# Kernel tuning notes

Hardware: AMD Instinct MI355X
Metric: run time of the kernel (lower is better)

## Reference

```python
import jax, jax.numpy as jnp
import numpy as np

B, T, V, D, H, C = 64, 512, 50000, 128, 256, 50


def setup_inputs() -> dict:
    key = jax.random.key(0)
    ks = jax.random.split(key, 15)
    s = 0.05
    rn = lambda k, shape: jax.random.normal(k, shape, jnp.float32) * s
    words = jax.random.randint(ks[0], (B, T), 0, V)
    target = jax.random.randint(ks[1], (B, T), 0, C)
    seq_len = jax.random.randint(ks[2], (B,), T // 2, T + 1)
    seq_len = seq_len.at[0].set(T)  # ensure at least one full-length sequence
    return dict(
        words=words, target=target, seq_len=seq_len,
        emb=rn(ks[3], (V, D)),
        W_ih_f=rn(ks[4], (4 * H, D)), W_hh_f=rn(ks[5], (4 * H, H)), b_f=rn(ks[6], (4 * H,)),
        W_ih_b=rn(ks[7], (4 * H, D)), W_hh_b=rn(ks[8], (4 * H, H)), b_b=rn(ks[9], (4 * H,)),
        fc_W=rn(ks[10], (C, 2 * H)), fc_b=rn(ks[11], (C,)),
        trans=rn(ks[12], (C, C)), start_s=rn(ks[13], (C,)), end_s=rn(ks[14], (C,)),
    )


def _lstm(x, W_ih, W_hh, b):
    # unidirectional LSTM, PyTorch gate order (i, f, g, o). x: [B,T,D] -> h: [B,T,H]
    Hh = W_hh.shape[1]
    xg = jnp.einsum('btd,gd->btg', x, W_ih) + b  # [B,T,4H]

    def step(carry, xt):
        h, c = carry
        g = xt + h @ W_hh.T
        i, f, gg, o = jnp.split(g, 4, axis=-1)
        c = jax.nn.sigmoid(f) * c + jax.nn.sigmoid(i) * jnp.tanh(gg)
        h = jax.nn.sigmoid(o) * jnp.tanh(c)
        return (h, c), h

    h0 = jnp.zeros((x.shape[0], Hh), x.dtype)
    _, hs = jax.lax.scan(step, (h0, h0), jnp.swapaxes(xg, 0, 1))
    return jnp.swapaxes(hs, 0, 1)


def _rev_idx(seq_len, t_len):
    # per-sequence time-reversal indices (packed-sequence semantics for the backward LSTM)
    t = jnp.arange(t_len)[None, :]
    L = seq_len[:, None]
    return jnp.where(t < L, L - 1 - t, t)


def _bilstm_crf_loss(words, target, seq_len, emb, W_ih_f, W_hh_f, b_f,
                     W_ih_b, W_hh_b, b_b, fc_W, fc_b, trans, start_s, end_s):
    x = emb[words]  # [B,T,D]
    h_f = _lstm(x, W_ih_f, W_hh_f, b_f)
    idx = _rev_idx(seq_len, x.shape[1])
    x_rev = jnp.take_along_axis(x, idx[:, :, None], axis=1)
    h_b = jnp.take_along_axis(_lstm(x_rev, W_ih_b, W_hh_b, b_b), idx[:, :, None], axis=1)
    feats = jnp.concatenate([h_f, h_b], axis=-1) @ fc_W.T + fc_b  # [B,T,C]
    logits = jax.nn.log_softmax(feats, axis=-1)
    mask = jnp.arange(x.shape[1])[None, :] < seq_len[:, None]  # [B,T] bool

    # --- CRF normalizer (forward algorithm) ---
    alpha0 = logits[:, 0] + start_s  # [B,C]

    def step(alpha, inp):
        emit_t, m_t = inp  # [B,C], [B]
        tmp = alpha[:, :, None] + trans[None, :, :] + emit_t[:, None, :]
        new = jax.nn.logsumexp(tmp, axis=1)
        return jnp.where(m_t[:, None], new, alpha), None

    alpha, _ = jax.lax.scan(step, alpha0,
                            (jnp.swapaxes(logits, 0, 1)[1:], jnp.swapaxes(mask, 0, 1)[1:]))
    norm = jax.nn.logsumexp(alpha + end_s, axis=1)  # [B]

    # --- gold path score ---
    maskf = mask.astype(logits.dtype)
    emit = jnp.take_along_axis(logits, target[:, :, None], axis=2)[..., 0]  # [B,T]
    trans_sc = trans[target[:, :-1], target[:, 1:]]  # [B,T-1]
    last = target[jnp.arange(target.shape[0]), seq_len - 1]
    gold = (emit * maskf).sum(1) + (trans_sc * maskf[:, 1:]).sum(1) \
           + start_s[target[:, 0]] + end_s[last]

    return jnp.mean(norm - gold)


def reference(words, target, seq_len, emb, W_ih_f, W_hh_f, b_f,
              W_ih_b, W_hh_b, b_b, fc_W, fc_b, trans, start_s, end_s):
    return _bilstm_crf_loss(words, target, seq_len, emb, W_ih_f, W_hh_f, b_f,
                            W_ih_b, W_hh_b, b_b, fc_W, fc_b, trans, start_s, end_s)
```

## Files before the change

kernel.cpp:

```cpp
#include <hip/hip_runtime.h>
#include <hip/hip_bf16.h>

#define BB 64
#define TT 512
#define DD 128
#define HH 256
#define G4 1024
#define CC 50

typedef __bf16 bf16x8 __attribute__((ext_vector_type(8)));
typedef float  f32x4  __attribute__((ext_vector_type(4)));
typedef _Float16 h16x2 __attribute__((ext_vector_type(2)));

#if defined(__has_builtin)
#if __has_builtin(__builtin_amdgcn_fdot2)
#define HAS_FDOT2 1
#endif
#endif

__device__ __forceinline__ float bl16(unsigned u) { return __uint_as_float(u << 16); }
__device__ __forceinline__ float bh16(unsigned u) { return __uint_as_float(u & 0xffff0000u); }

__device__ __forceinline__ float sigf(float x) {
    return 1.f / (1.f + __expf(-x));
}
__device__ __forceinline__ float tanh_s(float x) {
    float ax = fabsf(x);
    float e = __expf(-2.f * ax);
    float r = (1.f - e) / (1.f + e);
    return copysignf(r, x);
}

__device__ __forceinline__ float dot8(float acc, uint4 w, uint4 h) {
#ifdef HAS_FDOT2
    acc = __builtin_amdgcn_fdot2(__builtin_bit_cast(h16x2, w.x),
                                 __builtin_bit_cast(h16x2, h.x), acc, false);
    acc = __builtin_amdgcn_fdot2(__builtin_bit_cast(h16x2, w.y),
                                 __builtin_bit_cast(h16x2, h.y), acc, false);
    acc = __builtin_amdgcn_fdot2(__builtin_bit_cast(h16x2, w.z),
                                 __builtin_bit_cast(h16x2, h.z), acc, false);
    acc = __builtin_amdgcn_fdot2(__builtin_bit_cast(h16x2, w.w),
                                 __builtin_bit_cast(h16x2, h.w), acc, false);
#else
    {
        h16x2 a = __builtin_bit_cast(h16x2, w.x), b = __builtin_bit_cast(h16x2, h.x);
        acc = fmaf((float)a.x, (float)b.x, acc); acc = fmaf((float)a.y, (float)b.y, acc);
        a = __builtin_bit_cast(h16x2, w.y); b = __builtin_bit_cast(h16x2, h.y);
        acc = fmaf((float)a.x, (float)b.x, acc); acc = fmaf((float)a.y, (float)b.y, acc);
        a = __builtin_bit_cast(h16x2, w.z); b = __builtin_bit_cast(h16x2, h.z);
        acc = fmaf((float)a.x, (float)b.x, acc); acc = fmaf((float)a.y, (float)b.y, acc);
        a = __builtin_bit_cast(h16x2, w.w); b = __builtin_bit_cast(h16x2, h.w);
        acc = fmaf((float)a.x, (float)b.x, acc); acc = fmaf((float)a.y, (float)b.y, acc);
    }
#endif
    return acc;
}

__global__ __launch_bounds__(256) void k_cvt(
    const float* __restrict__ src, __hip_bfloat16* __restrict__ dst, int n)
{
    int i = (blockIdx.x * 256 + threadIdx.x) * 8;
    if (i + 8 <= n) {
        float4 a = *(const float4*)(src + i);
        float4 b = *(const float4*)(src + i + 4);
        __hip_bfloat16 o[8];
        o[0] = __float2bfloat16(a.x); o[1] = __float2bfloat16(a.y);
        o[2] = __float2bfloat16(a.z); o[3] = __float2bfloat16(a.w);
        o[4] = __float2bfloat16(b.x); o[5] = __float2bfloat16(b.y);
        o[6] = __float2bfloat16(b.z); o[7] = __float2bfloat16(b.w);
        *(uint4*)(dst + i) = *(const uint4*)o;
    }
}

__global__ __launch_bounds__(512) void k_pack(
    const float* __restrict__ Wf, const float* __restrict__ Wb,
    uint4* __restrict__ Wp)
{
    int blk = blockIdx.x;
    int half = blk & 1;
    int kc = (blk >> 1) & 31;
    int dir = blk >> 6;
    int j = threadIdx.x;
    int row = half * 512 + j;
    const float* src = (dir ? Wb : Wf) + (size_t)row * 256 + kc * 8;
    float4 a = *(const float4*)src;
    float4 b = *(const float4*)(src + 4);
    _Float16 o[8];
    o[0] = (_Float16)a.x; o[1] = (_Float16)a.y;
    o[2] = (_Float16)a.z; o[3] = (_Float16)a.w;
    o[4] = (_Float16)b.x; o[5] = (_Float16)b.y;
    o[6] = (_Float16)b.z; o[7] = (_Float16)b.w;
    Wp[((size_t)dir * 64 + kc * 2 + half) * 512 + j] = *(const uint4*)o;
}

__global__ __launch_bounds__(256, 2) void k_xg(
    const int* __restrict__ words,
    const float* __restrict__ embf,
    const __hip_bfloat16* __restrict__ Wih,
    const float* __restrict__ bfv, const float* __restrict__ bbv,
    __hip_bfloat16* __restrict__ xg)
{
    __shared__ __align__(16) __hip_bfloat16 A[64][136];
    int tid = threadIdx.x;
    int bt0 = blockIdx.x * 64;

    {
        int r = tid >> 2;
        int c0 = (tid & 3) * 32;
        int word = words[bt0 + r];
        const float* src = embf + (size_t)word * DD + c0;
#pragma unroll
        for (int i = 0; i < 8; ++i) {
            float4 v = *(const float4*)(src + i * 4);
            __hip_bfloat16 o[4] = {__float2bfloat16(v.x), __float2bfloat16(v.y),
                                   __float2bfloat16(v.z), __float2bfloat16(v.w)};
            *(uint2*)&A[r][c0 + i * 4] = *(const uint2*)o;
        }
    }
    __syncthreads();

    int wave = tid >> 6, lane = tid & 63;
    int m = lane & 15, quad = lane >> 4;

    bf16x8 afr[4][4];
#pragma unroll
    for (int ms = 0; ms < 4; ++ms)
#pragma unroll
        for (int kf = 0; kf < 4; ++kf)
            afr[ms][kf] = *(const bf16x8*)&A[ms * 16 + m][quad * 8 + kf * 32];

#pragma unroll 1
    for (int i = 0; i < 32; ++i) {
        int nt = wave * 32 + i;
        int gate_g = nt * 16 + m;
        int dir = gate_g >> 10;
        int gate = gate_g & 1023;
        const __hip_bfloat16* brow = Wih + (size_t)gate_g * DD + quad * 8;
        bf16x8 bfr[4];
#pragma unroll
        for (int kf = 0; kf < 4; ++kf) bfr[kf] = *(const bf16x8*)(brow + kf * 32);
        float bv = dir ? bbv[gate] : bfv[gate];
        size_t dbase = (size_t)dir * (size_t)(BB * TT * G4);

#pragma unroll
        for (int ms = 0; ms < 4; ++ms) {
            f32x4 acc = {0.f, 0.f, 0.f, 0.f};
#pragma unroll
            for (int kf = 0; kf < 4; ++kf)
                acc = __builtin_amdgcn_mfma_f32_16x16x32_bf16(afr[ms][kf], bfr[kf], acc, 0, 0, 0);
#pragma unroll
            for (int r = 0; r < 4; ++r) {
                int btrow = bt0 + ms * 16 + quad * 4 + r;
                xg[dbase + (size_t)btrow * G4 + gate] = __float2bfloat16(acc[r] + bv);
            }
        }
    }
}

__global__ __launch_bounds__(512)
__attribute__((amdgpu_waves_per_eu(2, 2)))
void k_lstm(
    const __hip_bfloat16* __restrict__ xg,
    const uint4* __restrict__ Wp,
    const int* __restrict__ seq_len,
    __hip_bfloat16* __restrict__ hcat)
{
    int b = blockIdx.x & 63;
    int dir = blockIdx.x >> 6;
    int j = threadIdx.x;

    __shared__ __align__(16) uint4 wB_lds[7 * 512];
    __shared__ float gbuf[2][512];
    __shared__ __align__(16) _Float16 hbf[2][HH];

    const uint4* Wd = Wp + (size_t)dir * 64 * 512;

    uint4 wA[32];
#pragma unroll
    for (int kc = 0; kc < 32; ++kc) wA[kc] = Wd[(kc * 2 + 0) * 512 + j];
    uint4 wB0[8];
#pragma unroll
    for (int kc = 0; kc < 8; ++kc) wB0[kc] = Wd[(kc * 2 + 1) * 512 + j];
#pragma unroll
    for (int kc = 8; kc < 15; ++kc) wB_lds[(kc - 8) * 512 + j] = Wd[(kc * 2 + 1) * 512 + j];

    if (j < HH) hbf[0][j] = (_Float16)0.f;
    float c = 0.f;
    int L = seq_len[b];
    const __hip_bfloat16* xgb = xg + (size_t)dir * (size_t)(BB * TT * G4)
                                   + (size_t)b * TT * G4;

    int tc = dir ? (L - 1) : 0;
    float xv0 = __bfloat162float(xgb[(size_t)tc * G4 + j]);
    float xv1 = __bfloat162float(xgb[(size_t)tc * G4 + 512 + j]);
    __syncthreads();

    for (int t = 0; t < TT; ++t) {
        int cur = t & 1, nxt = cur ^ 1;
        int tn = t + 1;
        int tcn = dir ? ((tn < L) ? (L - 1 - tn) : tn) : tn;
        bool pf = (tn < TT);
        __hip_bfloat16 p0, p1;
        if (pf) {
            p0 = xgb[(size_t)tcn * G4 + j];
            p1 = xgb[(size_t)tcn * G4 + 512 + j];
        }

        uint4 s1[9];
#pragma unroll
        for (int i = 0; i < 9; ++i) s1[i] = Wd[((15 + i) * 2 + 1) * 512 + j];

        const uint4* hv4 = (const uint4*)&hbf[cur][0];
        float a0 = 0.f, a1 = 0.f;
#pragma unroll
        for (int kc = 0; kc < 8; ++kc) {
            uint4 hv = hv4[kc];
            a0 = dot8(a0, wA[kc], hv);
            a1 = dot8(a1, wB0[kc], hv);
        }
#pragma unroll
        for (int kc = 8; kc < 15; ++kc) {
            uint4 hv = hv4[kc];
            a0 = dot8(a0, wA[kc], hv);
            a1 = dot8(a1, wB_lds[(kc - 8) * 512 + j], hv);
        }
        uint4 s2[8];
#pragma unroll
        for (int i = 0; i < 8; ++i) s2[i] = Wd[((24 + i) * 2 + 1) * 512 + j];
#pragma unroll
        for (int kc = 15; kc < 24; ++kc) {
            uint4 hv = hv4[kc];
            a0 = dot8(a0, wA[kc], hv);
            a1 = dot8(a1, s1[kc - 15], hv);
        }
#pragma unroll
        for (int kc = 24; kc < 32; ++kc) {
            uint4 hv = hv4[kc];
            a0 = dot8(a0, wA[kc], hv);
            a1 = dot8(a1, s2[kc - 24], hv);
        }
        gbuf[0][j] = a0 + xv0;
        gbuf[1][j] = a1 + xv1;
        __syncthreads();

        if (j < HH) {
            float gi = gbuf[0][j],      gg = gbuf[1][j];
            float gf = gbuf[0][HH + j], go = gbuf[1][HH + j];
            float i_ = sigf(gi), f_ = sigf(gf), G = tanh_s(gg), o_ = sigf(go);
            c = f_ * c + i_ * G;
            float h = o_ * tanh_s(c);
            hbf[nxt][j] = (_Float16)h;
            hcat[((size_t)(b * TT + tc)) * (2 * HH) + dir * HH + j] = __float2bfloat16(h);
        }
        if (pf) { xv0 = __bfloat162float(p0); xv1 = __bfloat162float(p1); }
        tc = tcn;
        __syncthreads();
    }
}

__global__ __launch_bounds__(64) void k_fc(
    const __hip_bfloat16* __restrict__ hcat,
    const __hip_bfloat16* __restrict__ fcW,
    const float* __restrict__ fcb,
    float* __restrict__ logits)
{
    int row = blockIdx.x;
    int tid = threadIdx.x;
    __shared__ __align__(16) float hrow[2 * HH];
    __shared__ float fbuf[CC + 2];

    {
        uint4 v = *(const uint4*)(hcat + (size_t)row * (2 * HH) + tid * 8);
        float* d = &hrow[tid * 8];
        d[0] = bl16(v.x); d[1] = bh16(v.x);
        d[2] = bl16(v.y); d[3] = bh16(v.y);
        d[4] = bl16(v.z); d[5] = bh16(v.z);
        d[6] = bl16(v.w); d[7] = bh16(v.w);
    }
    __syncthreads();

    if (tid < CC) {
        float acc = fcb[tid];
        const uint4* wr = (const uint4*)(fcW + (size_t)tid * (2 * HH));
#pragma unroll 8
        for (int kc = 0; kc < 64; ++kc) {
            uint4 wv = wr[kc];
            float4 h0 = *(const float4*)&hrow[kc * 8];
            float4 h1 = *(const float4*)&hrow[kc * 8 + 4];
            acc = fmaf(bl16(wv.x), h0.x, acc); acc = fmaf(bh16(wv.x), h0.y, acc);
            acc = fmaf(bl16(wv.y), h0.z, acc); acc = fmaf(bh16(wv.y), h0.w, acc);
            acc = fmaf(bl16(wv.z), h1.x, acc); acc = fmaf(bh16(wv.z), h1.y, acc);
            acc = fmaf(bl16(wv.w), h1.z, acc); acc = fmaf(bh16(wv.w), h1.w, acc);
        }
        fbuf[tid] = acc;
    }
    __syncthreads();

    float m = -1e30f;
    for (int i = 0; i < CC; ++i) m = fmaxf(m, fbuf[i]);
    float s = 0.f;
    for (int i = 0; i < CC; ++i) s += __expf(fbuf[i] - m);
    float lns = __logf(s);
    if (tid < CC) logits[(size_t)row * CC + tid] = fbuf[tid] - m - lns;
}

__global__ __launch_bounds__(256) void k_crf(
    const float* __restrict__ logits,
    const int* __restrict__ target,
    const int* __restrict__ seq_len,
    const float* __restrict__ trans,
    const float* __restrict__ start_s,
    const float* __restrict__ end_s,
    float* __restrict__ loss_b)
{
    const float L2E = 1.4426950408889634f;
    const float LN2 = 0.6931471805599453f;
    int b = blockIdx.x;
    int tid = threadIdx.x;
    int q = tid >> 6;
    int j = tid & 63;
    bool act = (j < CC);
    int L = seq_len[b];
    const float* lg = logits + (size_t)b * TT * CC;

    __shared__ float alpha2[64];
    __shared__ float mpart[4][64];
    __shared__ float spart[4][64];
    __shared__ float red[256];
    __shared__ float nbuf[CC + 2];

    int i0 = q * 13;
    int icnt = min(13, CC - i0);
    float treg[13];
    if (act) {
#pragma unroll
        for (int s = 0; s < 13; ++s)
            if (s < icnt) treg[s] = L2E * trans[(i0 + s) * CC + j];
    }
    if (q == 0 && act) alpha2[j] = L2E * (lg[j] + start_s[j]);
    __syncthreads();

    float v[13];
    for (int t = 1; t < L; ++t) {
        float mq = -1e30f;
        if (act) {
#pragma unroll
            for (int s = 0; s < 13; ++s)
                if (s < icnt) { v[s] = alpha2[i0 + s] + treg[s]; mq = fmaxf(mq, v[s]); }
        }
        mpart[q][j] = mq;
        __syncthreads();
        float M = fmaxf(fmaxf(mpart[0][j], mpart[1][j]), fmaxf(mpart[2][j], mpart[3][j]));
        float sq = 0.f;
        if (act) {
#pragma unroll
            for (int s = 0; s < 13; ++s)
                if (s < icnt) sq += exp2f(v[s] - M);
        }
        spart[q][j] = sq;
        __syncthreads();
        if (q == 0 && act) {
            float S = spart[0][j] + spart[1][j] + spart[2][j] + spart[3][j];
            alpha2[j] = M + log2f(S) + L2E * lg[(size_t)t * CC + j];
        }
        __syncthreads();
    }

    if (q == 0 && act) nbuf[j] = alpha2[j] + L2E * end_s[j];

    float gp = 0.f;
    const int* tg = target + b * TT;
    for (int t = tid; t < TT; t += 256) {
        if (t < L) {
            int c = tg[t];
            gp += lg[(size_t)t * CC + c];
            if (t >= 1) gp += trans[tg[t - 1] * CC + c];
        }
    }
    red[tid] = gp;
    __syncthreads();

    if (tid == 0) {
        float m2 = -1e30f;
        for (int i = 0; i < CC; ++i) m2 = fmaxf(m2, nbuf[i]);
        float s2 = 0.f;
        for (int i = 0; i < CC; ++i) s2 += exp2f(nbuf[i] - m2);
        float norm_nat = (m2 + log2f(s2)) * LN2;
        float g = 0.f;
        for (int i = 0; i < 256; ++i) g += red[i];
        g += start_s[tg[0]] + end_s[tg[L - 1]];
        loss_b[b] = norm_nat - g;
    }
}

__global__ void k_fin(const float* __restrict__ loss_b, float* __restrict__ out)
{
    int t = threadIdx.x;
    float v = loss_b[t];
#pragma unroll
    for (int o = 32; o > 0; o >>= 1) v += __shfl_down(v, o);
    if (t == 0) out[0] = v * (1.f / BB);
}

extern "C" void kernel_launch(void* const* d_in, const int* in_sizes, int n_in,
                              void* d_out, int out_size, void* d_ws, size_t ws_size,
                              hipStream_t stream)
{
    const int* words   = (const int*)d_in[0];
    const int* target  = (const int*)d_in[1];
    const int* seq_len = (const int*)d_in[2];
    const float* emb    = (const float*)d_in[3];
    const float* W_ih_f = (const float*)d_in[4];
    const float* W_hh_f = (const float*)d_in[5];
    const float* b_f    = (const float*)d_in[6];
    const float* W_ih_b = (const float*)d_in[7];
    const float* W_hh_b = (const float*)d_in[8];
    const float* b_b    = (const float*)d_in[9];
    const float* fc_W   = (const float*)d_in[10];
    const float* fc_b   = (const float*)d_in[11];
    const float* trans  = (const float*)d_in[12];
    const float* start_s= (const float*)d_in[13];
    const float* end_s  = (const float*)d_in[14];

    char* ws = (char*)d_ws;
    __hip_bfloat16* xg     = (__hip_bfloat16*)ws;
    __hip_bfloat16* hcat   = (__hip_bfloat16*)(ws + 134217728);
    float*          logits = (float*)(ws + 167772160);
    uint4*          Wp     = (uint4*)(ws + 167772160);
    float*          loss_b = (float*)(ws + 174325760);
    __hip_bfloat16* wihall = (__hip_bfloat16*)(ws + 174326016);
    __hip_bfloat16* fcw_bf = (__hip_bfloat16*)(ws + 174850304);

    k_cvt<<<64,  256, 0, stream>>>(W_ih_f, wihall,          131072);
    k_cvt<<<64,  256, 0, stream>>>(W_ih_b, wihall + 131072, 131072);
    k_cvt<<<13,  256, 0, stream>>>(fc_W,   fcw_bf,          25600);
    k_pack<<<128, 512, 0, stream>>>(W_hh_f, W_hh_b, Wp);

    k_xg  <<<512, 256, 0, stream>>>(words, emb, wihall, b_f, b_b, xg);
    k_lstm<<<128, 512, 0, stream>>>(xg, Wp, seq_len, hcat);
    k_fc  <<<32768, 64, 0, stream>>>(hcat, fcw_bf, fc_b, logits);
    k_crf <<<64, 256, 0, stream>>>(logits, target, seq_len, trans, start_s, end_s, loss_b);
    k_fin <<<1, 64, 0, stream>>>(loss_b, (float*)d_out);
}
```

Measured before the change: 1.889 ms.

## Compute all four LSTM gates per thread with 256-thread blocks

The recurrent LSTM kernel now runs 256 threads per block, and each thread computes all four gate pre-activations for one hidden unit. This removes the gbuf shared-memory exchange and one of the two barriers per timestep. W_hh is repacked into four gate groups: 26 of the 32 k-chunks are held in registers (104 uint4 per thread) and the remaining 6 sit in LDS, replacing the per-step global reloads of weight chunks. The trade-off is heavy register pressure at one wave per EU, half as many waves to hide latency, and four times the dot-product work per thread on the serial critical path.

```diff
diff --git a/kernel.cpp b/kernel.cpp
--- a/kernel.cpp
+++ b/kernel.cpp
@@ -72,16 +72,16 @@
     }
 }
 
-__global__ __launch_bounds__(512) void k_pack(
+__global__ __launch_bounds__(256) void k_pack(
     const float* __restrict__ Wf, const float* __restrict__ Wb,
     uint4* __restrict__ Wp)
 {
     int blk = blockIdx.x;
-    int half = blk & 1;
-    int kc = (blk >> 1) & 31;
-    int dir = blk >> 6;
+    int g   = blk & 3;
+    int kc  = (blk >> 2) & 31;
+    int dir = blk >> 7;
     int j = threadIdx.x;
-    int row = half * 512 + j;
+    int row = g * 256 + j;
     const float* src = (dir ? Wb : Wf) + (size_t)row * 256 + kc * 8;
     float4 a = *(const float4*)src;
     float4 b = *(const float4*)(src + 4);
@@ -90,7 +90,7 @@
     o[2] = (_Float16)a.z; o[3] = (_Float16)a.w;
     o[4] = (_Float16)b.x; o[5] = (_Float16)b.y;
     o[6] = (_Float16)b.z; o[7] = (_Float16)b.w;
-    Wp[((size_t)dir * 64 + kc * 2 + half) * 512 + j] = *(const uint4*)o;
+    Wp[((size_t)(dir * 32 + kc) * 4 + g) * 256 + j] = *(const uint4*)o;
 }
 
 __global__ __launch_bounds__(256, 2) void k_xg(
@@ -157,8 +157,8 @@
     }
 }
 
-__global__ __launch_bounds__(512)
-__attribute__((amdgpu_waves_per_eu(2, 2)))
+__global__ __launch_bounds__(256)
+__attribute__((amdgpu_waves_per_eu(1, 1)))
 void k_lstm(
     const __hip_bfloat16* __restrict__ xg,
     const uint4* __restrict__ Wp,
@@ -169,22 +169,25 @@
     int dir = blockIdx.x >> 6;
     int j = threadIdx.x;
 
-    __shared__ __align__(16) uint4 wB_lds[7 * 512];
-    __shared__ float gbuf[2][512];
+    __shared__ __align__(16) uint4 wlds[6 * 4 * 256];
     __shared__ __align__(16) _Float16 hbf[2][HH];
 
-    const uint4* Wd = Wp + (size_t)dir * 64 * 512;
-
-    uint4 wA[32];
-#pragma unroll
-    for (int kc = 0; kc < 32; ++kc) wA[kc] = Wd[(kc * 2 + 0) * 512 + j];
-    uint4 wB0[8];
-#pragma unroll
-    for (int kc = 0; kc < 8; ++kc) wB0[kc] = Wd[(kc * 2 + 1) * 512 + j];
-#pragma unroll
-    for (int kc = 8; kc < 15; ++kc) wB_lds[(kc - 8) * 512 + j] = Wd[(kc * 2 + 1) * 512 + j];
-
-    if (j < HH) hbf[0][j] = (_Float16)0.f;
+    const uint4* Wd = Wp + (size_t)dir * (32 * 4 * 256);
+
+    uint4 wr[26][4];
+#pragma unroll
+    for (int kc = 0; kc < 26; ++kc)
+#pragma unroll
+        for (int g = 0; g < 4; ++g)
+            wr[kc][g] = Wd[(kc * 4 + g) * 256 + j];
+
+#pragma unroll
+    for (int kc = 26; kc < 32; ++kc)
+#pragma unroll
+        for (int g = 0; g < 4; ++g)
+            wlds[((kc - 26) * 4 + g) * 256 + j] = Wd[(kc * 4 + g) * 256 + j];
+
+    hbf[0][j] = (_Float16)0.f;
     float c = 0.f;
     int L = seq_len[b];
     const __hip_bfloat16* xgb = xg + (size_t)dir * (size_t)(BB * TT * G4)
@@ -192,7 +195,9 @@
 
     int tc = dir ? (L - 1) : 0;
     float xv0 = __bfloat162float(xgb[(size_t)tc * G4 + j]);
-    float xv1 = __bfloat162float(xgb[(size_t)tc * G4 + 512 + j]);
+    float xv1 = __bfloat162float(xgb[(size_t)tc * G4 + 256 + j]);
+    float xv2 = __bfloat162float(xgb[(size_t)tc * G4 + 512 + j]);
+    float xv3 = __bfloat162float(xgb[(size_t)tc * G4 + 768 + j]);
     __syncthreads();
 
     for (int t = 0; t < TT; ++t) {
@@ -200,59 +205,45 @@
         int tn = t + 1;
         int tcn = dir ? ((tn < L) ? (L - 1 - tn) : tn) : tn;
         bool pf = (tn < TT);
-        __hip_bfloat16 p0, p1;
+        __hip_bfloat16 p0, p1, p2, p3;
         if (pf) {
-            p0 = xgb[(size_t)tcn * G4 + j];
-            p1 = xgb[(size_t)tcn * G4 + 512 + j];
-        }
-
-        uint4 s1[9];
-#pragma unroll
-        for (int i = 0; i < 9; ++i) s1[i] = Wd[((15 + i) * 2 + 1) * 512 + j];
+            const __hip_bfloat16* xr = xgb + (size_t)tcn * G4 + j;
+            p0 = xr[0]; p1 = xr[256]; p2 = xr[512]; p3 = xr[768];
+        }
 
         const uint4* hv4 = (const uint4*)&hbf[cur][0];
-        float a0 = 0.f, a1 = 0.f;
-#pragma unroll
-        for (int kc = 0; kc < 8; ++kc) {
+        float a0 = 0.f, a1 = 0.f, a2 = 0.f, a3 = 0.f;
+#pragma unroll
+        for (int kc = 0; kc < 26; ++kc) {
             uint4 hv = hv4[kc];
-            a0 = dot8(a0, wA[kc], hv);
-            a1 = dot8(a1, wB0[kc], hv);
-        }
-#pragma unroll
-        for (int kc = 8; kc < 15; ++kc) {
+            a0 = dot8(a0, wr[kc][0], hv);
+            a1 = dot8(a1, wr[kc][1], hv);
+            a2 = dot8(a2, wr[kc][2], hv);
+            a3 = dot8(a3, wr[kc][3], hv);
+        }
+#pragma unroll
+        for (int kc = 26; kc < 32; ++kc) {
             uint4 hv = hv4[kc];
-            a0 = dot8(a0, wA[kc], hv);
-            a1 = dot8(a1, wB_lds[(kc - 8) * 512 + j], hv);
-        }
-        uint4 s2[8];
-#pragma unroll
-        for (int i = 0; i < 8; ++i) s2[i] = Wd[((24 + i) * 2 + 1) * 512 + j];
-#pragma unroll
-        for (int kc = 15; kc < 24; ++kc) {
-            uint4 hv = hv4[kc];
-            a0 = dot8(a0, wA[kc], hv);
-            a1 = dot8(a1, s1[kc - 15], hv);
-        }
-#pragma unroll
-        for (int kc = 24; kc < 32; ++kc) {
-            uint4 hv = hv4[kc];
-            a0 = dot8(a0, wA[kc], hv);
-            a1 = dot8(a1, s2[kc - 24], hv);
-        }
-        gbuf[0][j] = a0 + xv0;
-        gbuf[1][j] = a1 + xv1;
-        __syncthreads();
-
-        if (j < HH) {
-            float gi = gbuf[0][j],      gg = gbuf[1][j];
-            float gf = gbuf[0][HH + j], go = gbuf[1][HH + j];
-            float i_ = sigf(gi), f_ = sigf(gf), G = tanh_s(gg), o_ = sigf(go);
-            c = f_ * c + i_ * G;
-            float h = o_ * tanh_s(c);
-            hbf[nxt][j] = (_Float16)h;
-            hcat[((size_t)(b * TT + tc)) * (2 * HH) + dir * HH + j] = __float2bfloat16(h);
-        }
-        if (pf) { xv0 = __bfloat162float(p0); xv1 = __bfloat162float(p1); }
+            const uint4* wl = &wlds[((kc - 26) * 4) * 256 + j];
+            a0 = dot8(a0, wl[0],   hv);
+            a1 = dot8(a1, wl[256], hv);
+            a2 = dot8(a2, wl[512], hv);
+            a3 = dot8(a3, wl[768], hv);
+        }
+
+        float i_ = sigf(a0 + xv0);
+        float f_ = sigf(a1 + xv1);
+        float G  = tanh_s(a2 + xv2);
+        float o_ = sigf(a3 + xv3);
+        c = f_ * c + i_ * G;
+        float h = o_ * tanh_s(c);
+        hbf[nxt][j] = (_Float16)h;
+        hcat[((size_t)(b * TT + tc)) * (2 * HH) + dir * HH + j] = __float2bfloat16(h);
+
+        if (pf) {
+            xv0 = __bfloat162float(p0); xv1 = __bfloat162float(p1);
+            xv2 = __bfloat162float(p2); xv3 = __bfloat162float(p3);
+        }
         tc = tcn;
         __syncthreads();
     }
@@ -434,10 +425,10 @@
     k_cvt<<<64,  256, 0, stream>>>(W_ih_f, wihall,          131072);
     k_cvt<<<64,  256, 0, stream>>>(W_ih_b, wihall + 131072, 131072);
     k_cvt<<<13,  256, 0, stream>>>(fc_W,   fcw_bf,          25600);
-    k_pack<<<128, 512, 0, stream>>>(W_hh_f, W_hh_b, Wp);
+    k_pack<<<256, 256, 0, stream>>>(W_hh_f, W_hh_b, Wp);
 
     k_xg  <<<512, 256, 0, stream>>>(words, emb, wihall, b_f, b_b, xg);
-    k_lstm<<<128, 512, 0, stream>>>(xg, Wp, seq_len, hcat);
+    k_lstm<<<128, 256, 0, stream>>>(xg, Wp, seq_len, hcat);
     k_fc  <<<32768, 64, 0, stream>>>(hcat, fcw_bf, fc_b, logits);
     k_crf <<<64, 256, 0, stream>>>(logits, target, seq_len, trans, start_s, end_s, loss_b);
     k_fin <<<1, 64, 0, stream>>>(loss_b, (float*)d_out);
```

Measured after the change: 2.488 ms. 1.32x slower.
